# Kernel tuning notes

Hardware: AMD Instinct MI355X
Metric: run time of the kernel (lower is better)

## Reference

```python
import jax, jax.numpy as jnp
import numpy as np

U, I, D = 100000, 50000, 64
ALPHA = 0.2  # tf.nn.leaky_relu default


def seg_softmax(v, seg, n):
    # sparse row-wise softmax (tf.sparse.softmax equivalent)
    m = jax.ops.segment_max(v, seg, num_segments=n)
    e = jnp.exp(v - m[seg])
    s = jax.ops.segment_sum(e, seg, num_segments=n)
    return e / (s[seg] + 1e-12)


def spmm(att, row, col, x, n):
    # sparse_dense_matmul: out[r] = sum_e att[e] * x[col[e]]
    return jax.ops.segment_sum(att[:, None] * x[col], row, num_segments=n)


def edge_logit(raw, w, b):
    # Dense(1, sigmoid) on per-edge scalar, then exp (pre sparse-softmax)
    return jnp.exp(jax.nn.sigmoid(raw * w + b))


def graph_att(x, W, b1, w2, b2):
    # Dense(1, tanh) -> Dense(1, leaky_relu) on concat embeddings [N, 2D]
    h = jnp.tanh(x @ W + b1)  # [N]
    return jax.nn.leaky_relu(h * w2 + b2, ALPHA)


def setup_inputs() -> dict:
    key = jax.random.key(0)
    ks = jax.random.split(key, 24)
    Es, Eui, Eiu, B = 800000, 1000000, 1000000, 4096
    f32 = jnp.float32
    inp = {
        'user_embedding': jax.random.normal(ks[0], (U, D), f32) * 0.01,
        'item_embedding': jax.random.normal(ks[1], (I, D), f32) * 0.01,
        'snii1': jax.random.normal(ks[2], (Es,), f32),
        'snii2': jax.random.normal(ks[3], (Es,), f32),
        'ciii1': jax.random.normal(ks[4], (Eui,), f32),
        'ciii2': jax.random.normal(ks[5], (Eui,), f32),
        'icii1': jax.random.normal(ks[6], (Eiu,), f32),
        'icii2': jax.random.normal(ks[7], (Eiu,), f32) * 0.01,
        'low_att_w': jax.random.normal(ks[8], (6,), f32),
        'low_att_b': jax.random.normal(ks[9], (6,), f32),
        'att1_W': jax.random.normal(ks[10], (8, 2 * D), f32) * 0.1,
        'att1_b': jax.random.normal(ks[11], (8,), f32) * 0.1,
        'att2_w': jax.random.normal(ks[12], (8,), f32),
        'att2_b': jax.random.normal(ks[13], (8,), f32) * 0.1,
        'sn_row': jax.random.randint(ks[14], (Es,), 0, U, jnp.int32),
        'sn_col': jax.random.randint(ks[15], (Es,), 0, U, jnp.int32),
        'ci_row': jax.random.randint(ks[16], (Eui,), 0, U, jnp.int32),
        'ci_col': jax.random.randint(ks[17], (Eui,), 0, I, jnp.int32),
        'ic_row': jax.random.randint(ks[18], (Eiu,), 0, I, jnp.int32),
        'ic_col': jax.random.randint(ks[19], (Eiu,), 0, U, jnp.int32),
        'user_idx': jax.random.randint(ks[20], (B,), 0, U, jnp.int32),
        'item_idx': jax.random.randint(ks[21], (B,), 0, I, jnp.int32),
    }
    return inp


def reference(user_embedding, item_embedding, snii1, snii2, ciii1, ciii2,
              icii1, icii2, low_att_w, low_att_b, att1_W, att1_b, att2_w, att2_b,
              sn_row, sn_col, ci_row, ci_col, ic_row, ic_col, user_idx, item_idx):
    # low-level attention-weighted adjacency matrices (sparse softmax per row)
    sn1 = seg_softmax(edge_logit(snii1, low_att_w[0], low_att_b[0]), sn_row, U)
    sn2 = seg_softmax(edge_logit(snii2, low_att_w[1], low_att_b[1]), sn_row, U)
    ci1 = seg_softmax(edge_logit(ciii1, low_att_w[2], low_att_b[2]), ci_row, U)
    ci2 = seg_softmax(edge_logit(ciii2, low_att_w[3], low_att_b[3]), ci_row, U)
    ic1 = seg_softmax(edge_logit(icii1, low_att_w[4], low_att_b[4]), ic_row, I)
    ic2 = seg_softmax(edge_logit(icii2, low_att_w[5], low_att_b[5]), ic_row, I)

    u0, i0 = user_embedding, item_embedding

    def user_layer(u, it, att_sn, att_ci, k):
        u_from_i = spmm(att_ci, ci_row, ci_col, it, U)
        u_from_u = spmm(att_sn, sn_row, sn_col, u, U)
        a_int = jnp.exp(graph_att(jnp.concatenate([u, u_from_i], 1), att1_W[k], att1_b[k], att2_w[k], att2_b[k])) + 0.7
        a_soc = jnp.exp(graph_att(jnp.concatenate([u, u_from_u], 1), att1_W[k + 1], att1_b[k + 1], att2_w[k + 1], att2_b[k + 1])) + 0.3
        s = a_int + a_soc
        return 0.5 * u + 0.5 * ((a_int / s)[:, None] * u_from_i + (a_soc / s)[:, None] * u_from_u)

    def item_layer(u, it, att_ic, k):
        i_from_u = spmm(att_ic, ic_row, ic_col, u, I)
        a_self = jnp.exp(graph_att(jnp.concatenate([it, it], 1), att1_W[k], att1_b[k], att2_w[k], att2_b[k])) + 1.0
        a_cust = jnp.exp(graph_att(jnp.concatenate([it, i_from_u], 1), att1_W[k + 1], att1_b[k + 1], att2_w[k + 1], att2_b[k + 1])) + 1.0
        s = a_self + a_cust
        return (a_self / s)[:, None] * it + (a_cust / s)[:, None] * i_from_u

    u1 = user_layer(u0, i0, sn1, ci1, 0)
    i1 = item_layer(u0, i0, ic1, 4)
    u2 = user_layer(u1, i1, sn2, ci2, 2)
    i2 = item_layer(u1, i1, ic2, 6)

    fu = jnp.concatenate([u0, u1, u2], 1)  # [U, 3D]
    fi = jnp.concatenate([i0, i1, i2], 1)  # [I, 3D]
    return jax.nn.sigmoid(jnp.sum(fu[user_idx] * fi[item_idx], axis=1))  # [B]
```

## Files before the change

kernel.cpp:

```cpp
#include <hip/hip_runtime.h>
#include <math.h>

#define DIM 64
#define NBLK 512
#define NTHR 1024
#define KMAX 4096
#define NSEG 8
#define SEGW (NBLK / NSEG)

typedef unsigned short ushort_t;
typedef unsigned int uint_t;
typedef unsigned char uchar_t;
typedef float v2f __attribute__((ext_vector_type(2)));

__device__ __forceinline__ ushort_t f2bf(float f) {
    uint_t u = __float_as_uint(f);
    return (ushort_t)((u + 0x7fffu + ((u >> 16) & 1u)) >> 16);
}


__global__ void count_cvt_kernel(const float* __restrict__ u0, const float* __restrict__ i0,
                                 uchar_t* __restrict__ ub, uchar_t* __restrict__ ib,
                                 size_t n8u, size_t n8t,
                                 const int* __restrict__ sn_row, const int* __restrict__ ci_row,
                                 const int* __restrict__ ic_row, int* __restrict__ cntBlk,
                                 int Es, int Eui, int Eiu, int U, int K) {
    __shared__ int h[KMAX];
    int b = blockIdx.x, tid = threadIdx.x;
    size_t gtid = (size_t)b * NTHR + tid;
    const size_t GT = (size_t)NBLK * NTHR;

    for (size_t i = gtid; i < n8t; i += GT) {
        const float4* src; uchar_t* dst; size_t di;
        if (i < n8u) { src = (const float4*)u0; dst = ub; di = i; }
        else         { src = (const float4*)i0; dst = ib; di = i - n8u; }
        float4 a = src[2 * di], c = src[2 * di + 1];
        int lo = 0, hi = 0;
        lo = __builtin_amdgcn_cvt_pk_fp8_f32(a.x * 256.0f, a.y * 256.0f, lo, false);
        lo = __builtin_amdgcn_cvt_pk_fp8_f32(a.z * 256.0f, a.w * 256.0f, lo, true);
        hi = __builtin_amdgcn_cvt_pk_fp8_f32(c.x * 256.0f, c.y * 256.0f, hi, false);
        hi = __builtin_amdgcn_cvt_pk_fp8_f32(c.z * 256.0f, c.w * 256.0f, hi, true);
        ((uint2*)dst)[di] = make_uint2((uint_t)lo, (uint_t)hi);
    }

    int E = Es + Eui + Eiu;
    int per = (E + NBLK - 1) / NBLK;
    int e0 = b * per, e1 = min(e0 + per, E);
    for (int i = tid; i < K; i += NTHR) h[i] = 0;
    __syncthreads();
    for (int e = e0 + tid; e < e1; e += NTHR) {
        int r;
        if (e < Es) r = sn_row[e];
        else if (e < Es + Eui) r = U + ci_row[e - Es];
        else r = 2 * U + ic_row[e - Es - Eui];
        atomicAdd(&h[r >> 6], 1);
    }
    __syncthreads();
    for (int i = tid; i < K; i += NTHR) cntBlk[(size_t)b * K + i] = h[i];
}


__global__ void base1_kernel(const int* __restrict__ cntBlk, int* __restrict__ baseBlk,
                             int* __restrict__ segsum, int K) {
    int k = blockIdx.x * 256 + threadIdx.x;
    int s = blockIdx.y;
    if (k >= K) return;
    int b0 = s * SEGW;
    int acc = 0;
    #pragma unroll 8
    for (int j = 0; j < SEGW; j++) {
        baseBlk[(size_t)(b0 + j) * K + k] = acc;
        acc += cntBlk[(size_t)(b0 + j) * K + k];
    }
    segsum[(size_t)s * K + k] = acc;
}


__global__ void scan_kernel(const int* __restrict__ segsum, int* __restrict__ segoff,
                            int* __restrict__ bucketPtr, int K, int E) {
    __shared__ int sums[NTHR];
    int tid = threadIdx.x;
    const int CH = KMAX / NTHR;
    int loc[CH];
    int base0 = tid * CH, s = 0;
    #pragma unroll
    for (int j = 0; j < CH; j++) {
        int idx = base0 + j;
        int tot = 0;
        if (idx < K) {
            #pragma unroll
            for (int sg = 0; sg < NSEG; sg++) {
                segoff[(size_t)sg * K + idx] = tot;
                tot += segsum[(size_t)sg * K + idx];
            }
        }
        loc[j] = s; s += tot;
    }
    sums[tid] = s;
    __syncthreads();
    for (int off = 1; off < NTHR; off <<= 1) {
        int t = 0;
        if (tid >= off) t = sums[tid - off];
        __syncthreads();
        if (tid >= off) sums[tid] += t;
        __syncthreads();
    }
    int offs = (tid > 0) ? sums[tid - 1] : 0;
    #pragma unroll
    for (int j = 0; j < CH; j++) {
        int idx = base0 + j;
        if (idx < K) bucketPtr[idx] = offs + loc[j];
    }
    if (tid == 0) bucketPtr[K] = E;
}


__global__ void place_kernel(const int* __restrict__ sn_row, const int* __restrict__ sn_col,
                             const int* __restrict__ ci_row, const int* __restrict__ ci_col,
                             const int* __restrict__ ic_row, const int* __restrict__ ic_col,
                             const float* __restrict__ snii1, const float* __restrict__ snii2,
                             const float* __restrict__ ciii1, const float* __restrict__ ciii2,
                             const float* __restrict__ icii1, const float* __restrict__ icii2,
                             const float* __restrict__ lw, const float* __restrict__ lb,
                             const int* __restrict__ bucketPtr, const int* __restrict__ segoff,
                             const int* __restrict__ baseBlk, uint2* __restrict__ barr,
                             int Es, int Eui, int Eiu, int U, int K) {
    __shared__ int cur[KMAX];
    int E = Es + Eui + Eiu;
    int per = (E + NBLK - 1) / NBLK;
    int b = blockIdx.x;
    int sb = b / SEGW;
    int e0 = b * per, e1 = min(e0 + per, E);
    for (int i = threadIdx.x; i < K; i += NTHR)
        cur[i] = bucketPtr[i] + segoff[(size_t)sb * K + i] + baseBlk[(size_t)b * K + i];
    __syncthreads();
    for (int e = e0 + threadIdx.x; e < e1; e += NTHR) {
        int r, c, j1, j2;
        float r1, r2;
        if (e < Es) {
            r = sn_row[e]; c = sn_col[e]; r1 = snii1[e]; r2 = snii2[e]; j1 = 0; j2 = 1;
        } else if (e < Es + Eui) {
            int t = e - Es;
            r = U + ci_row[t]; c = ci_col[t]; r1 = ciii1[t]; r2 = ciii2[t]; j1 = 2; j2 = 3;
        } else {
            int t = e - Es - Eui;
            r = 2 * U + ic_row[t]; c = ic_col[t]; r1 = icii1[t]; r2 = icii2[t]; j1 = 4; j2 = 5;
        }
        float t1 = expf(expf(1.0f / (1.0f + expf(-(r1 * lw[j1] + lb[j1])))));
        float t2 = expf(expf(1.0f / (1.0f + expf(-(r2 * lw[j2] + lb[j2])))));
        uint_t packed = (uint_t)f2bf(t1) | ((uint_t)f2bf(t2) << 16);
        int k = r >> 6;
        int pos = atomicAdd(&cur[k], 1);
        barr[pos] = make_uint2(((uint_t)(r & 63) << 26) | (uint_t)c, packed);
    }
}


__global__ void finalize_kernel(const uint2* __restrict__ barr, const int* __restrict__ bucketPtr,
                                int* __restrict__ ptr, uint2* __restrict__ rec,
                                int R, int K, int E) {
    __shared__ int h[64], sc[64], cur2[64];
    int k = blockIdx.x;
    int s0 = bucketPtr[k], s1 = bucketPtr[k + 1];
    if (threadIdx.x < 64) { h[threadIdx.x] = 0; cur2[threadIdx.x] = 0; }
    __syncthreads();
    for (int e = s0 + threadIdx.x; e < s1; e += blockDim.x)
        atomicAdd(&h[(int)(barr[e].x >> 26)], 1);
    __syncthreads();
    if (threadIdx.x < 64) {
        int v = h[threadIdx.x];
        int inc = v;
        #pragma unroll
        for (int off = 1; off < 64; off <<= 1) {
            int t = __shfl_up(inc, off, 64);
            if (threadIdx.x >= off) inc += t;
        }
        sc[threadIdx.x] = inc - v;
        int r = k * 64 + threadIdx.x;
        if (r < R) ptr[r] = s0 + inc - v;
    }
    if (k == K - 1 && threadIdx.x == 0) ptr[R] = E;
    __syncthreads();
    for (int e = s0 + threadIdx.x; e < s1; e += blockDim.x) {
        uint2 q = barr[e];
        int r6 = (int)(q.x >> 26);
        int rank = atomicAdd(&cur2[r6], 1);
        rec[s0 + sc[r6] + rank] = make_uint2(q.x & 0x3ffffffu, q.y);
    }
}


__device__ __forceinline__ float att_scalar(float dot, float b1, float w2, float b2, float addc) {
    float h = tanhf(dot + b1);
    float z = h * w2 + b2;
    float lr = z > 0.0f ? z : 0.2f * z;
    return expf(lr) + addc;
}

__device__ __forceinline__ void fp8_fma8v(v2f acc[4], uint2 v, float a) {
    v2f av = {a, a};
    acc[0] += av * __builtin_amdgcn_cvt_pk_f32_fp8((int)v.x, false);
    acc[1] += av * __builtin_amdgcn_cvt_pk_f32_fp8((int)v.x, true);
    acc[2] += av * __builtin_amdgcn_cvt_pk_f32_fp8((int)v.y, false);
    acc[3] += av * __builtin_amdgcn_cvt_pk_f32_fp8((int)v.y, true);
}

__device__ __forceinline__ float dot8_lanes(float d) {
    #pragma unroll
    for (int off = 1; off < 8; off <<= 1) d += __shfl_xor(d, off, 64);
    return d;
}

__device__ __forceinline__ void agg_row8(const uint2* __restrict__ rec, const uchar_t* __restrict__ tab,
                                         int e0, int e1, int l8, int lanebase,
                                         v2f acc[4], float& s) {
    if (e0 >= e1) return;
    int last = e1 - 1;
    int idx0 = e0 + l8;
    uint2 t0 = rec[min(idx0, last)];
    uint2 q;
    q.x = (idx0 <= last) ? t0.x : 0u;
    q.y = (idx0 <= last) ? t0.y : 0u;
    for (int base = e0; base < e1; base += 8) {
        int nidx = base + 8 + l8;
        uint2 tn = rec[min(nidx, last)];
        uint2 qn;
        qn.x = (nidx <= last) ? tn.x : 0u;
        qn.y = (nidx <= last) ? tn.y : 0u;
        s += __uint_as_float(q.y << 16);
        #pragma unroll
        for (int j = 0; j < 8; j++) {
            uint_t cx = __shfl(q.x, lanebase + j, 64);
            uint_t wy = __shfl(q.y, lanebase + j, 64);
            float a = __uint_as_float(wy << 16);
            uint2 v = ((const uint2*)(tab + (size_t)cx * DIM))[l8];
            fp8_fma8v(acc, v, a);
        }
        q = qn;
    }
}

__global__ void layer1_kernel(const uchar_t* __restrict__ ub8, const uchar_t* __restrict__ ib8,
                              const float* __restrict__ u0, const float* __restrict__ i0,
                              const int* __restrict__ ptr, const uint2* __restrict__ rec,
                              const float* __restrict__ W1, const float* __restrict__ b1v,
                              const float* __restrict__ w2v, const float* __restrict__ b2v,
                              float* __restrict__ u1, float* __restrict__ i1, int U, int I) {
    int gid = blockIdx.x * (blockDim.x >> 3) + (threadIdx.x >> 3);
    int lane = threadIdx.x & 63;
    int l8 = lane & 7;
    int lanebase = lane & 56;
    if (gid >= U + I) return;
    bool is_user = gid < U;
    int r = is_user ? gid : gid - U;

    v2f A[4]  = {{0.f, 0.f}, {0.f, 0.f}, {0.f, 0.f}, {0.f, 0.f}};
    v2f Bv[4] = {{0.f, 0.f}, {0.f, 0.f}, {0.f, 0.f}, {0.f, 0.f}};
    float s_a = 0.f, s_b = 0.f;

    if (is_user) {
        agg_row8(rec, ib8, ptr[U + r], ptr[U + r + 1], l8, lanebase, A, s_a);
        agg_row8(rec, ub8, ptr[r], ptr[r + 1], l8, lanebase, Bv, s_b);
    } else {
        agg_row8(rec, ub8, ptr[2 * U + r], ptr[2 * U + r + 1], l8, lanebase, A, s_a);
    }
    s_a = dot8_lanes(s_a);
    s_b = dot8_lanes(s_b);

    float ka = (1.0f / (s_a + 1e-12f)) * 0.00390625f;
    float kb = (1.0f / (s_b + 1e-12f)) * 0.00390625f;
    float ac[8], bc[8];
    #pragma unroll
    for (int j = 0; j < 4; j++) {
        ac[2 * j] = A[j][0] * ka;  ac[2 * j + 1] = A[j][1] * ka;
        bc[2 * j] = Bv[j][0] * kb; bc[2 * j + 1] = Bv[j][1] * kb;
    }

    const float* selfp = (is_user ? u0 : i0) + (size_t)r * DIM + 8 * l8;
    float4 s0 = *(const float4*)selfp;
    float4 s1 = *(const float4*)(selfp + 4);
    float sf[8] = {s0.x, s0.y, s0.z, s0.w, s1.x, s1.y, s1.z, s1.w};
    int k = is_user ? 0 : 4;
    const float* Wa = W1 + k * 2 * DIM;
    const float* Wb = Wa + 2 * DIM;
    float d1 = 0.f, d2 = 0.f;
    #pragma unroll
    for (int j = 0; j < 8; j++) {
        float wa0 = Wa[8 * l8 + j], wa1 = Wa[DIM + 8 * l8 + j];
        float wb0 = Wb[8 * l8 + j], wb1 = Wb[DIM + 8 * l8 + j];
        if (is_user) {
            d1 += sf[j] * wa0 + ac[j] * wa1;
            d2 += sf[j] * wb0 + bc[j] * wb1;
        } else {
            d1 += sf[j] * (wa0 + wa1);
            d2 += sf[j] * wb0 + ac[j] * wb1;
        }
    }
    d1 = dot8_lanes(d1);
    d2 = dot8_lanes(d2);

    float out8[8];
    float* op;
    if (is_user) {
        float a_int = att_scalar(d1, b1v[0], w2v[0], b2v[0], 0.7f);
        float a_soc = att_scalar(d2, b1v[1], w2v[1], b2v[1], 0.3f);
        float sg = a_int + a_soc;
        float wi = a_int / sg, ws = a_soc / sg;
        #pragma unroll
        for (int j = 0; j < 8; j++)
            out8[j] = 0.5f * sf[j] + 0.5f * (wi * ac[j] + ws * bc[j]);
        op = u1 + (size_t)r * DIM + 8 * l8;
    } else {
        float a_self = att_scalar(d1, b1v[4], w2v[4], b2v[4], 1.0f);
        float a_cust = att_scalar(d2, b1v[5], w2v[5], b2v[5], 1.0f);
        float sg = a_self + a_cust;
        float wi = a_self / sg, ws = a_cust / sg;
        #pragma unroll
        for (int j = 0; j < 8; j++)
            out8[j] = wi * sf[j] + ws * ac[j];
        op = i1 + (size_t)r * DIM + 8 * l8;
    }
    *(float4*)op = make_float4(out8[0], out8[1], out8[2], out8[3]);
    *(float4*)(op + 4) = make_float4(out8[4], out8[5], out8[6], out8[7]);
}

__global__ void layer2_kernel(const float* __restrict__ u1, const float* __restrict__ i1,
                              const int* __restrict__ ptr, const uint2* __restrict__ rec,
                              const float* __restrict__ W1, const float* __restrict__ b1v,
                              const float* __restrict__ w2v, const float* __restrict__ b2v,
                              const int* __restrict__ uidx, const int* __restrict__ iidx,
                              float* __restrict__ u2s, float* __restrict__ i2s, int U, int B) {
    int wid = blockIdx.x * (blockDim.x >> 6) + (threadIdx.x >> 6);
    int lane = threadIdx.x & 63;
    if (wid >= 2 * B) return;
    int g = lane >> 3, l8 = lane & 7;
    bool is_user = wid < B;
    int b = is_user ? wid : wid - B;
    int r = is_user ? uidx[b] : iidx[b];

    float acc_a[8] = {0, 0, 0, 0, 0, 0, 0, 0};
    float acc_b[8] = {0, 0, 0, 0, 0, 0, 0, 0};
    float s_a = 0.f, s_b = 0.f;

    if (is_user) {
        int e0 = ptr[U + r], e1 = ptr[U + r + 1];
        for (int e = e0 + g; e < e1; e += 8) {
            uint2 q = rec[e];
            float a = __uint_as_float(q.y & 0xffff0000u);
            s_a += a;
            const float4* rp = (const float4*)(i1 + (size_t)q.x * DIM);
            float4 v0 = rp[2 * l8], v1 = rp[2 * l8 + 1];
            acc_a[0] = fmaf(a, v0.x, acc_a[0]); acc_a[1] = fmaf(a, v0.y, acc_a[1]);
            acc_a[2] = fmaf(a, v0.z, acc_a[2]); acc_a[3] = fmaf(a, v0.w, acc_a[3]);
            acc_a[4] = fmaf(a, v1.x, acc_a[4]); acc_a[5] = fmaf(a, v1.y, acc_a[5]);
            acc_a[6] = fmaf(a, v1.z, acc_a[6]); acc_a[7] = fmaf(a, v1.w, acc_a[7]);
        }
        e0 = ptr[r]; e1 = ptr[r + 1];
        for (int e = e0 + g; e < e1; e += 8) {
            uint2 q = rec[e];
            float a = __uint_as_float(q.y & 0xffff0000u);
            s_b += a;
            const float4* rp = (const float4*)(u1 + (size_t)q.x * DIM);
            float4 v0 = rp[2 * l8], v1 = rp[2 * l8 + 1];
            acc_b[0] = fmaf(a, v0.x, acc_b[0]); acc_b[1] = fmaf(a, v0.y, acc_b[1]);
            acc_b[2] = fmaf(a, v0.z, acc_b[2]); acc_b[3] = fmaf(a, v0.w, acc_b[3]);
            acc_b[4] = fmaf(a, v1.x, acc_b[4]); acc_b[5] = fmaf(a, v1.y, acc_b[5]);
            acc_b[6] = fmaf(a, v1.z, acc_b[6]); acc_b[7] = fmaf(a, v1.w, acc_b[7]);
        }
    } else {
        int e0 = ptr[2 * U + r], e1 = ptr[2 * U + r + 1];
        for (int e = e0 + g; e < e1; e += 8) {
            uint2 q = rec[e];
            float a = __uint_as_float(q.y & 0xffff0000u);
            s_a += a;
            const float4* rp = (const float4*)(u1 + (size_t)q.x * DIM);
            float4 v0 = rp[2 * l8], v1 = rp[2 * l8 + 1];
            acc_a[0] = fmaf(a, v0.x, acc_a[0]); acc_a[1] = fmaf(a, v0.y, acc_a[1]);
            acc_a[2] = fmaf(a, v0.z, acc_a[2]); acc_a[3] = fmaf(a, v0.w, acc_a[3]);
            acc_a[4] = fmaf(a, v1.x, acc_a[4]); acc_a[5] = fmaf(a, v1.y, acc_a[5]);
            acc_a[6] = fmaf(a, v1.z, acc_a[6]); acc_a[7] = fmaf(a, v1.w, acc_a[7]);
        }
    }

    #pragma unroll
    for (int off = 8; off < 64; off <<= 1) {
        s_a += __shfl_xor(s_a, off, 64);
        #pragma unroll
        for (int j = 0; j < 8; j++) acc_a[j] += __shfl_xor(acc_a[j], off, 64);
    }
    if (is_user) {
        #pragma unroll
        for (int off = 8; off < 64; off <<= 1) {
            s_b += __shfl_xor(s_b, off, 64);
            #pragma unroll
            for (int j = 0; j < 8; j++) acc_b[j] += __shfl_xor(acc_b[j], off, 64);
        }
    }
    float ka = 1.0f / (s_a + 1e-12f);
    float kb = 1.0f / (s_b + 1e-12f);

    if (g == 0) {
        #pragma unroll
        for (int j = 0; j < 8; j++) { acc_a[j] *= ka; acc_b[j] *= kb; }
        const float* selfp = (is_user ? u1 : i1) + (size_t)r * DIM + 8 * l8;
        float4 s0 = *(const float4*)selfp;
        float4 s1 = *(const float4*)(selfp + 4);
        float sf[8] = {s0.x, s0.y, s0.z, s0.w, s1.x, s1.y, s1.z, s1.w};
        int k = is_user ? 2 : 6;
        const float* Wa = W1 + k * 2 * DIM;
        const float* Wb = Wa + 2 * DIM;
        float d1 = 0.f, d2 = 0.f;
        #pragma unroll
        for (int j = 0; j < 8; j++) {
            float wa0 = Wa[8 * l8 + j], wa1 = Wa[DIM + 8 * l8 + j];
            float wb0 = Wb[8 * l8 + j], wb1 = Wb[DIM + 8 * l8 + j];
            if (is_user) {
                d1 += sf[j] * wa0 + acc_a[j] * wa1;
                d2 += sf[j] * wb0 + acc_b[j] * wb1;
            } else {
                d1 += sf[j] * (wa0 + wa1);
                d2 += sf[j] * wb0 + acc_a[j] * wb1;
            }
        }
        d1 = dot8_lanes(d1);
        d2 = dot8_lanes(d2);

        float out8[8];
        float* op;
        if (is_user) {
            float a_int = att_scalar(d1, b1v[2], w2v[2], b2v[2], 0.7f);
            float a_soc = att_scalar(d2, b1v[3], w2v[3], b2v[3], 0.3f);
            float sg = a_int + a_soc;
            float wi = a_int / sg, ws = a_soc / sg;
            #pragma unroll
            for (int j = 0; j < 8; j++)
                out8[j] = 0.5f * sf[j] + 0.5f * (wi * acc_a[j] + ws * acc_b[j]);
            op = u2s + (size_t)b * DIM + 8 * l8;
        } else {
            float a_self = att_scalar(d1, b1v[6], w2v[6], b2v[6], 1.0f);
            float a_cust = att_scalar(d2, b1v[7], w2v[7], b2v[7], 1.0f);
            float sg = a_self + a_cust;
            float wi = a_self / sg, ws = a_cust / sg;
            #pragma unroll
            for (int j = 0; j < 8; j++)
                out8[j] = wi * sf[j] + ws * acc_a[j];
            op = i2s + (size_t)b * DIM + 8 * l8;
        }
        *(float4*)op = make_float4(out8[0], out8[1], out8[2], out8[3]);
        *(float4*)(op + 4) = make_float4(out8[4], out8[5], out8[6], out8[7]);
    }
}


__global__ void final_kernel(const float* __restrict__ u0, const float* __restrict__ u1,
                             const float* __restrict__ u2s,
                             const float* __restrict__ i0, const float* __restrict__ i1,
                             const float* __restrict__ i2s,
                             const int* __restrict__ uidx, const int* __restrict__ iidx,
                             float* __restrict__ out, int n) {
    int b = blockIdx.x * (blockDim.x >> 6) + (threadIdx.x >> 6);
    int lane = threadIdx.x & 63;
    if (b >= n) return;
    size_t ur = (size_t)uidx[b] * DIM + lane;
    size_t ir = (size_t)iidx[b] * DIM + lane;
    size_t sr = (size_t)b * DIM + lane;
    float acc = u0[ur] * i0[ir] + u1[ur] * i1[ir] + u2s[sr] * i2s[sr];
    #pragma unroll
    for (int off = 32; off > 0; off >>= 1) acc += __shfl_xor(acc, off, 64);
    if (lane == 0) out[b] = 1.0f / (1.0f + expf(-acc));
}


extern "C" void kernel_launch(void* const* d_in, const int* in_sizes, int n_in,
                              void* d_out, int out_size, void* d_ws, size_t ws_size,
                              hipStream_t stream) {
    const float* user_emb = (const float*)d_in[0];
    const float* item_emb = (const float*)d_in[1];
    const float* snii1 = (const float*)d_in[2];
    const float* snii2 = (const float*)d_in[3];
    const float* ciii1 = (const float*)d_in[4];
    const float* ciii2 = (const float*)d_in[5];
    const float* icii1 = (const float*)d_in[6];
    const float* icii2 = (const float*)d_in[7];
    const float* low_w = (const float*)d_in[8];
    const float* low_b = (const float*)d_in[9];
    const float* att1_W = (const float*)d_in[10];
    const float* att1_b = (const float*)d_in[11];
    const float* att2_w = (const float*)d_in[12];
    const float* att2_b = (const float*)d_in[13];
    const int* sn_row = (const int*)d_in[14];
    const int* sn_col = (const int*)d_in[15];
    const int* ci_row = (const int*)d_in[16];
    const int* ci_col = (const int*)d_in[17];
    const int* ic_row = (const int*)d_in[18];
    const int* ic_col = (const int*)d_in[19];
    const int* user_idx = (const int*)d_in[20];
    const int* item_idx = (const int*)d_in[21];
    float* out = (float*)d_out;

    const int Es  = in_sizes[2];
    const int Eui = in_sizes[4];
    const int Eiu = in_sizes[6];
    const int U = in_sizes[0] / DIM;
    const int I = in_sizes[1] / DIM;
    const int B = in_sizes[20];
    const int R = 2 * U + I;
    const int E = Es + Eui + Eiu;
    const int K = (R + 63) >> 6;

    char* wsb = (char*)d_ws;
    size_t off = 0;
    auto alloc = [&](size_t n_units) {
        off = (off + 3) & ~(size_t)3;
        void* p = wsb + off * 4; off += n_units; return p;
    };

    int* cntBlk    = (int*)alloc((size_t)NBLK * K);
    int* baseBlk   = (int*)alloc((size_t)NBLK * K);
    int* segsum    = (int*)alloc((size_t)NSEG * K);
    int* segoff    = (int*)alloc((size_t)NSEG * K);
    int* bucketPtr = (int*)alloc(K + 1);
    int* ptr       = (int*)alloc(R + 1);
    uint2* barr    = (uint2*)alloc((size_t)E * 2);
    uint2* rec     = (uint2*)alloc((size_t)E * 2);
    uchar_t* ub8 = (uchar_t*)alloc((size_t)U * DIM / 4);
    uchar_t* ib8 = (uchar_t*)alloc((size_t)I * DIM / 4);
    float* u1  = (float*)alloc((size_t)U * DIM);
    float* i1  = (float*)alloc((size_t)I * DIM);
    float* u2s = (float*)alloc((size_t)B * DIM);
    float* i2s = (float*)alloc((size_t)B * DIM);
    (void)ws_size;

    size_t n8u = (size_t)U * DIM / 8, n8t = (size_t)(U + I) * DIM / 8;

    count_cvt_kernel<<<NBLK, NTHR, 0, stream>>>(user_emb, item_emb, ub8, ib8, n8u, n8t,
                                                sn_row, ci_row, ic_row, cntBlk,
                                                Es, Eui, Eiu, U, K);
    base1_kernel<<<dim3((K + 255) / 256, NSEG), 256, 0, stream>>>(cntBlk, baseBlk, segsum, K);
    scan_kernel<<<1, NTHR, 0, stream>>>(segsum, segoff, bucketPtr, K, E);
    place_kernel<<<NBLK, NTHR, 0, stream>>>(sn_row, sn_col, ci_row, ci_col, ic_row, ic_col,
                                            snii1, snii2, ciii1, ciii2, icii1, icii2,
                                            low_w, low_b, bucketPtr, segoff, baseBlk, barr,
                                            Es, Eui, Eiu, U, K);
    finalize_kernel<<<K, 256, 0, stream>>>(barr, bucketPtr, ptr, rec, R, K, E);

    layer1_kernel<<<(U + I + 31) / 32, 256, 0, stream>>>(ub8, ib8, user_emb, item_emb,
        ptr, rec, att1_W, att1_b, att2_w, att2_b, u1, i1, U, I);

    layer2_kernel<<<(2 * B + 3) / 4, 256, 0, stream>>>(u1, i1, ptr, rec,
        att1_W, att1_b, att2_w, att2_b, user_idx, item_idx, u2s, i2s, U, B);

    final_kernel<<<(B + 3) / 4, 256, 0, stream>>>(user_emb, u1, u2s, item_emb, i1, i2s,
                                                  user_idx, item_idx, out, B);
}
```

Measured before the change: 334.1 us.

## Compute per-row degrees with global atomics and scan them to build CSR pointers

The counting pass now also accumulates per-row degrees with global atomics, using vectorized int4 row loads and a grid-stride loop over each edge list in place of the contiguous per-block chunking. A multi-block two-pass scan over the degrees produces the row pointers directly. Bucket offsets are then derived from those pointers, and the finalize pass no longer needs its per-bucket histogram and scan. The placement kernel also uses vectorized loads per edge list. In exchange the count pass issues many global atomics, there are extra launches and a memset, and the bucket regions each block handles are no longer contiguous.

```diff
diff --git a/kernel.cpp b/kernel.cpp
--- a/kernel.cpp
+++ b/kernel.cpp
@@ -7,6 +7,7 @@
 #define KMAX 4096
 #define NSEG 8
 #define SEGW (NBLK / NSEG)
+#define SCH  4096
 
 typedef unsigned short ushort_t;
 typedef unsigned int uint_t;
@@ -18,12 +19,36 @@
     return (ushort_t)((u + 0x7fffu + ((u >> 16) & 1u)) >> 16);
 }
 
+
+__device__ __forceinline__ void count_list(const int* __restrict__ rows, int EL, int base,
+                                           int* h, int* __restrict__ deg,
+                                           size_t gtid, size_t GT) {
+    size_t nq = ((size_t)EL + 3) >> 2;
+    for (size_t q = gtid; q < nq; q += GT) {
+        int e = (int)(q << 2);
+        if (e + 4 <= EL) {
+            int4 r4 = *(const int4*)(rows + e);
+            int v0 = base + r4.x, v1 = base + r4.y, v2 = base + r4.z, v3 = base + r4.w;
+            atomicAdd(&h[v0 >> 6], 1); atomicAdd(&h[v1 >> 6], 1);
+            atomicAdd(&h[v2 >> 6], 1); atomicAdd(&h[v3 >> 6], 1);
+            atomicAdd(&deg[v0], 1); atomicAdd(&deg[v1], 1);
+            atomicAdd(&deg[v2], 1); atomicAdd(&deg[v3], 1);
+        } else {
+            for (int j = e; j < EL; j++) {
+                int v = base + rows[j];
+                atomicAdd(&h[v >> 6], 1);
+                atomicAdd(&deg[v], 1);
+            }
+        }
+    }
+}
 
 __global__ void count_cvt_kernel(const float* __restrict__ u0, const float* __restrict__ i0,
                                  uchar_t* __restrict__ ub, uchar_t* __restrict__ ib,
                                  size_t n8u, size_t n8t,
                                  const int* __restrict__ sn_row, const int* __restrict__ ci_row,
                                  const int* __restrict__ ic_row, int* __restrict__ cntBlk,
+                                 int* __restrict__ deg,
                                  int Es, int Eui, int Eiu, int U, int K) {
     __shared__ int h[KMAX];
     int b = blockIdx.x, tid = threadIdx.x;
@@ -43,18 +68,11 @@
         ((uint2*)dst)[di] = make_uint2((uint_t)lo, (uint_t)hi);
     }
 
-    int E = Es + Eui + Eiu;
-    int per = (E + NBLK - 1) / NBLK;
-    int e0 = b * per, e1 = min(e0 + per, E);
     for (int i = tid; i < K; i += NTHR) h[i] = 0;
     __syncthreads();
-    for (int e = e0 + tid; e < e1; e += NTHR) {
-        int r;
-        if (e < Es) r = sn_row[e];
-        else if (e < Es + Eui) r = U + ci_row[e - Es];
-        else r = 2 * U + ic_row[e - Es - Eui];
-        atomicAdd(&h[r >> 6], 1);
-    }
+    count_list(sn_row, Es, 0, h, deg, gtid, GT);
+    count_list(ci_row, Eui, U, h, deg, gtid, GT);
+    count_list(ic_row, Eiu, 2 * U, h, deg, gtid, GT);
     __syncthreads();
     for (int i = tid; i < K; i += NTHR) cntBlk[(size_t)b * K + i] = h[i];
 }
@@ -76,25 +94,18 @@
 }
 
 
-__global__ void scan_kernel(const int* __restrict__ segsum, int* __restrict__ segoff,
-                            int* __restrict__ bucketPtr, int K, int E) {
+__global__ void scan1_kernel(const int* __restrict__ deg, int* __restrict__ tmp,
+                             int* __restrict__ bsum, int R) {
     __shared__ int sums[NTHR];
-    int tid = threadIdx.x;
-    const int CH = KMAX / NTHR;
-    int loc[CH];
-    int base0 = tid * CH, s = 0;
-    #pragma unroll
-    for (int j = 0; j < CH; j++) {
+    int tid = threadIdx.x, b = blockIdx.x;
+    int base0 = b * SCH + tid * 4;
+    int loc[4];
+    int s = 0;
+    #pragma unroll
+    for (int j = 0; j < 4; j++) {
         int idx = base0 + j;
-        int tot = 0;
-        if (idx < K) {
-            #pragma unroll
-            for (int sg = 0; sg < NSEG; sg++) {
-                segoff[(size_t)sg * K + idx] = tot;
-                tot += segsum[(size_t)sg * K + idx];
-            }
-        }
-        loc[j] = s; s += tot;
+        int v = (idx < R) ? deg[idx] : 0;
+        loc[j] = s; s += v;
     }
     sums[tid] = s;
     __syncthreads();
@@ -107,13 +118,83 @@
     }
     int offs = (tid > 0) ? sums[tid - 1] : 0;
     #pragma unroll
-    for (int j = 0; j < CH; j++) {
+    for (int j = 0; j < 4; j++) {
         int idx = base0 + j;
-        if (idx < K) bucketPtr[idx] = offs + loc[j];
-    }
-    if (tid == 0) bucketPtr[K] = E;
-}
-
+        if (idx < R) tmp[idx] = offs + loc[j];
+    }
+    if (tid == NTHR - 1) bsum[b] = sums[NTHR - 1];
+}
+
+
+__global__ void ptr_kernel(const int* __restrict__ tmp, const int* __restrict__ bsum,
+                           int* __restrict__ ptr, int R, int E) {
+    __shared__ int soff;
+    int b = blockIdx.x, tid = threadIdx.x;
+    if (tid < 64) {
+        int v = (tid < b) ? bsum[tid] : 0;
+        #pragma unroll
+        for (int o = 32; o > 0; o >>= 1) v += __shfl_xor(v, o, 64);
+        if (tid == 0) soff = v;
+    }
+    __syncthreads();
+    int off = soff;
+    int base0 = b * SCH + tid * 4;
+    #pragma unroll
+    for (int j = 0; j < 4; j++) {
+        int idx = base0 + j;
+        if (idx < R) ptr[idx] = tmp[idx] + off;
+    }
+    if (b == 0 && tid == 0) ptr[R] = E;
+}
+
+
+__global__ void segoff_kernel(const int* __restrict__ segsum, const int* __restrict__ ptr,
+                              int* __restrict__ segoff, int* __restrict__ bucketPtr, int K) {
+    int k = blockIdx.x * 256 + threadIdx.x;
+    if (k >= K) return;
+    int tot = 0;
+    #pragma unroll
+    for (int sg = 0; sg < NSEG; sg++) {
+        segoff[(size_t)sg * K + k] = tot;
+        tot += segsum[(size_t)sg * K + k];
+    }
+    bucketPtr[k] = ptr[64 * k];
+}
+
+
+__device__ __forceinline__ void place_edge(int v, int c, float r1, float r2,
+                                           float w1, float b1, float w2, float b2,
+                                           int* cur, uint2* __restrict__ barr) {
+    float t1 = expf(expf(1.0f / (1.0f + expf(-(r1 * w1 + b1)))));
+    float t2 = expf(expf(1.0f / (1.0f + expf(-(r2 * w2 + b2)))));
+    uint_t packed = (uint_t)f2bf(t1) | ((uint_t)f2bf(t2) << 16);
+    int pos = atomicAdd(&cur[v >> 6], 1);
+    barr[pos] = make_uint2(((uint_t)(v & 63) << 26) | (uint_t)c, packed);
+}
+
+__device__ __forceinline__ void place_list(const int* __restrict__ rows, const int* __restrict__ cols,
+                                           const float* __restrict__ x1, const float* __restrict__ x2,
+                                           int EL, int base, float w1, float b1, float w2, float b2,
+                                           int* cur, uint2* __restrict__ barr,
+                                           size_t gtid, size_t GT) {
+    size_t nq = ((size_t)EL + 3) >> 2;
+    for (size_t q = gtid; q < nq; q += GT) {
+        int e = (int)(q << 2);
+        if (e + 4 <= EL) {
+            int4 r4 = *(const int4*)(rows + e);
+            int4 c4 = *(const int4*)(cols + e);
+            float4 a4 = *(const float4*)(x1 + e);
+            float4 b4 = *(const float4*)(x2 + e);
+            place_edge(base + r4.x, c4.x, a4.x, b4.x, w1, b1, w2, b2, cur, barr);
+            place_edge(base + r4.y, c4.y, a4.y, b4.y, w1, b1, w2, b2, cur, barr);
+            place_edge(base + r4.z, c4.z, a4.z, b4.z, w1, b1, w2, b2, cur, barr);
+            place_edge(base + r4.w, c4.w, a4.w, b4.w, w1, b1, w2, b2, cur, barr);
+        } else {
+            for (int j = e; j < EL; j++)
+                place_edge(base + rows[j], cols[j], x1[j], x2[j], w1, b1, w2, b2, cur, barr);
+        }
+    }
+}
 
 __global__ void place_kernel(const int* __restrict__ sn_row, const int* __restrict__ sn_col,
                              const int* __restrict__ ci_row, const int* __restrict__ ci_col,
@@ -126,66 +207,36 @@
                              const int* __restrict__ baseBlk, uint2* __restrict__ barr,
                              int Es, int Eui, int Eiu, int U, int K) {
     __shared__ int cur[KMAX];
-    int E = Es + Eui + Eiu;
-    int per = (E + NBLK - 1) / NBLK;
     int b = blockIdx.x;
     int sb = b / SEGW;
-    int e0 = b * per, e1 = min(e0 + per, E);
+    size_t gtid = (size_t)b * NTHR + threadIdx.x;
+    const size_t GT = (size_t)NBLK * NTHR;
     for (int i = threadIdx.x; i < K; i += NTHR)
         cur[i] = bucketPtr[i] + segoff[(size_t)sb * K + i] + baseBlk[(size_t)b * K + i];
     __syncthreads();
-    for (int e = e0 + threadIdx.x; e < e1; e += NTHR) {
-        int r, c, j1, j2;
-        float r1, r2;
-        if (e < Es) {
-            r = sn_row[e]; c = sn_col[e]; r1 = snii1[e]; r2 = snii2[e]; j1 = 0; j2 = 1;
-        } else if (e < Es + Eui) {
-            int t = e - Es;
-            r = U + ci_row[t]; c = ci_col[t]; r1 = ciii1[t]; r2 = ciii2[t]; j1 = 2; j2 = 3;
-        } else {
-            int t = e - Es - Eui;
-            r = 2 * U + ic_row[t]; c = ic_col[t]; r1 = icii1[t]; r2 = icii2[t]; j1 = 4; j2 = 5;
-        }
-        float t1 = expf(expf(1.0f / (1.0f + expf(-(r1 * lw[j1] + lb[j1])))));
-        float t2 = expf(expf(1.0f / (1.0f + expf(-(r2 * lw[j2] + lb[j2])))));
-        uint_t packed = (uint_t)f2bf(t1) | ((uint_t)f2bf(t2) << 16);
-        int k = r >> 6;
-        int pos = atomicAdd(&cur[k], 1);
-        barr[pos] = make_uint2(((uint_t)(r & 63) << 26) | (uint_t)c, packed);
-    }
-}
-
-
-__global__ void finalize_kernel(const uint2* __restrict__ barr, const int* __restrict__ bucketPtr,
-                                int* __restrict__ ptr, uint2* __restrict__ rec,
-                                int R, int K, int E) {
-    __shared__ int h[64], sc[64], cur2[64];
+    place_list(sn_row, sn_col, snii1, snii2, Es, 0,     lw[0], lb[0], lw[1], lb[1], cur, barr, gtid, GT);
+    place_list(ci_row, ci_col, ciii1, ciii2, Eui, U,    lw[2], lb[2], lw[3], lb[3], cur, barr, gtid, GT);
+    place_list(ic_row, ic_col, icii1, icii2, Eiu, 2 * U, lw[4], lb[4], lw[5], lb[5], cur, barr, gtid, GT);
+}
+
+
+__global__ void finalize_kernel(const uint2* __restrict__ barr, const int* __restrict__ ptr,
+                                uint2* __restrict__ rec, int R, int K) {
+    __shared__ int cur2[64];
     int k = blockIdx.x;
-    int s0 = bucketPtr[k], s1 = bucketPtr[k + 1];
-    if (threadIdx.x < 64) { h[threadIdx.x] = 0; cur2[threadIdx.x] = 0; }
+    int r0 = k * 64;
+    if (threadIdx.x < 64) {
+        int r = r0 + threadIdx.x;
+        cur2[threadIdx.x] = (r < R) ? ptr[r] : 0;
+    }
     __syncthreads();
-    for (int e = s0 + threadIdx.x; e < s1; e += blockDim.x)
-        atomicAdd(&h[(int)(barr[e].x >> 26)], 1);
-    __syncthreads();
-    if (threadIdx.x < 64) {
-        int v = h[threadIdx.x];
-        int inc = v;
-        #pragma unroll
-        for (int off = 1; off < 64; off <<= 1) {
-            int t = __shfl_up(inc, off, 64);
-            if (threadIdx.x >= off) inc += t;
-        }
-        sc[threadIdx.x] = inc - v;
-        int r = k * 64 + threadIdx.x;
-        if (r < R) ptr[r] = s0 + inc - v;
-    }
-    if (k == K - 1 && threadIdx.x == 0) ptr[R] = E;
-    __syncthreads();
-    for (int e = s0 + threadIdx.x; e < s1; e += blockDim.x) {
+    int s0 = ptr[r0];
+    int s1 = ptr[min(r0 + 64, R)];
+    for (int e = s0 + (int)threadIdx.x; e < s1; e += (int)blockDim.x) {
         uint2 q = barr[e];
         int r6 = (int)(q.x >> 26);
-        int rank = atomicAdd(&cur2[r6], 1);
-        rec[s0 + sc[r6] + rank] = make_uint2(q.x & 0x3ffffffu, q.y);
+        int pos = atomicAdd(&cur2[r6], 1);
+        rec[pos] = make_uint2(q.x & 0x3ffffffu, q.y);
     }
 }
 
@@ -507,6 +558,7 @@
     const int R = 2 * U + I;
     const int E = Es + Eui + Eiu;
     const int K = (R + 63) >> 6;
+    const int NCH = (R + SCH - 1) / SCH;
 
     char* wsb = (char*)d_ws;
     size_t off = 0;
@@ -519,7 +571,10 @@
     int* baseBlk   = (int*)alloc((size_t)NBLK * K);
     int* segsum    = (int*)alloc((size_t)NSEG * K);
     int* segoff    = (int*)alloc((size_t)NSEG * K);
-    int* bucketPtr = (int*)alloc(K + 1);
+    int* bucketPtr = (int*)alloc(K);
+    int* deg       = (int*)alloc(R);
+    int* tmp       = (int*)alloc(R);
+    int* bsum      = (int*)alloc(64);
     int* ptr       = (int*)alloc(R + 1);
     uint2* barr    = (uint2*)alloc((size_t)E * 2);
     uint2* rec     = (uint2*)alloc((size_t)E * 2);
@@ -533,16 +588,19 @@
 
     size_t n8u = (size_t)U * DIM / 8, n8t = (size_t)(U + I) * DIM / 8;
 
+    hipMemsetAsync(deg, 0, sizeof(int) * (size_t)R, stream);
     count_cvt_kernel<<<NBLK, NTHR, 0, stream>>>(user_emb, item_emb, ub8, ib8, n8u, n8t,
-                                                sn_row, ci_row, ic_row, cntBlk,
+                                                sn_row, ci_row, ic_row, cntBlk, deg,
                                                 Es, Eui, Eiu, U, K);
     base1_kernel<<<dim3((K + 255) / 256, NSEG), 256, 0, stream>>>(cntBlk, baseBlk, segsum, K);
-    scan_kernel<<<1, NTHR, 0, stream>>>(segsum, segoff, bucketPtr, K, E);
+    scan1_kernel<<<NCH, NTHR, 0, stream>>>(deg, tmp, bsum, R);
+    ptr_kernel<<<NCH, NTHR, 0, stream>>>(tmp, bsum, ptr, R, E);
+    segoff_kernel<<<(K + 255) / 256, 256, 0, stream>>>(segsum, ptr, segoff, bucketPtr, K);
     place_kernel<<<NBLK, NTHR, 0, stream>>>(sn_row, sn_col, ci_row, ci_col, ic_row, ic_col,
                                             snii1, snii2, ciii1, ciii2, icii1, icii2,
                                             low_w, low_b, bucketPtr, segoff, baseBlk, barr,
                                             Es, Eui, Eiu, U, K);
-    finalize_kernel<<<K, 256, 0, stream>>>(barr, bucketPtr, ptr, rec, R, K, E);
+    finalize_kernel<<<K, 256, 0, stream>>>(barr, ptr, rec, R, K);
 
     layer1_kernel<<<(U + I + 31) / 32, 256, 0, stream>>>(ub8, ib8, user_emb, item_emb,
         ptr, rec, att1_W, att1_b, att2_w, att2_b, u1, i1, U, I);
```

Measured after the change: 420.4 us. 25.8% more time.
